# Optimization experiments

Hardware: AMD Instinct MI355X
Metric: run time of the kernel (lower is better)

Reference implementation:

```python
import jax, jax.numpy as jnp
import numpy as np

N = 50000      # nodes
E = 800000     # directed edges (before self-loops)
IN = 128       # in_channels
H = 4          # heads (layers 1,2)
C = 64         # hidden_channels per head
OUT = 512      # out_channels of final Linear
LEAKY_SLOPE = 0.2


def _gat_layer(x, src, dst, n, W, a_src, a_dst, b, concat):
    """PyG GATConv (v1): shared linear, additive attention, segment softmax over dst."""
    heads, ch = a_src.shape
    xl = (x @ W).reshape(n, heads, ch)                       # [N,H,C]
    as_n = jnp.sum(xl * a_src, axis=-1)                      # [N,H] alpha_src per node
    ad_n = jnp.sum(xl * a_dst, axis=-1)                      # [N,H] alpha_dst per node
    logits = jax.nn.leaky_relu(as_n[src] + ad_n[dst], LEAKY_SLOPE)  # [Etot,H]
    m = jax.lax.stop_gradient(jax.ops.segment_max(logits, dst, num_segments=n))
    p = jnp.exp(logits - m[dst])
    denom = jax.ops.segment_sum(p, dst, num_segments=n) + 1e-16
    alpha = p / denom[dst]                                   # segment softmax over incoming edges
    out = jax.ops.segment_sum(xl[src] * alpha[:, :, None], dst, num_segments=n)  # [N,H,C]
    out = out.reshape(n, heads * ch) if concat else out.mean(axis=1)
    return out + b


def setup_inputs() -> dict:
    key = jax.random.key(0)
    ks = jax.random.split(key, 16)

    def gl(k, shape, fan_in):
        return jax.random.normal(k, shape, dtype=jnp.float32) * np.float32(1.0 / np.sqrt(fan_in))

    x = jax.random.normal(ks[0], (N, IN), dtype=jnp.float32)
    edge_index = jax.random.randint(ks[1], (2, E), 0, N, dtype=jnp.int32)

    inp = {
        "x": x,
        "edge_index": edge_index,
        # layer 1: in -> H*C (concat)
        "W1": gl(ks[2], (IN, H * C), IN),
        "a_src1": gl(ks[3], (H, C), C),
        "a_dst1": gl(ks[4], (H, C), C),
        "b1": jnp.zeros((H * C,), jnp.float32),
        # layer 2: H*C -> H*C (concat)
        "W2": gl(ks[5], (H * C, H * C), H * C),
        "a_src2": gl(ks[6], (H, C), C),
        "a_dst2": gl(ks[7], (H, C), C),
        "b2": jnp.zeros((H * C,), jnp.float32),
        # layer 3: H*C -> C (1 head, no concat)
        "W3": gl(ks[8], (H * C, C), H * C),
        "a_src3": gl(ks[9], (1, C), C),
        "a_dst3": gl(ks[10], (1, C), C),
        "b3": jnp.zeros((C,), jnp.float32),
        # final fc: C -> OUT
        "Wfc": gl(ks[11], (C, OUT), C),
        "bfc": jnp.zeros((OUT,), jnp.float32),
    }
    return inp


def reference(x, edge_index, W1, a_src1, a_dst1, b1, W2, a_src2, a_dst2, b2,
              W3, a_src3, a_dst3, b3, Wfc, bfc):
    n = x.shape[0]
    loop = jnp.arange(n, dtype=edge_index.dtype)             # PyG GATConv adds self-loops
    src = jnp.concatenate([edge_index[0], loop])
    dst = jnp.concatenate([edge_index[1], loop])

    h = jax.nn.relu(_gat_layer(x, src, dst, n, W1, a_src1, a_dst1, b1, True))
    h = jax.nn.relu(_gat_layer(h, src, dst, n, W2, a_src2, a_dst2, b2, True))
    h = jax.nn.relu(_gat_layer(h, src, dst, n, W3, a_src3, a_dst3, b3, False))
    return jax.nn.relu(h @ Wfc + bfc)                        # [N, OUT]
```

## Files before the change

### kernel.cpp

```cpp
#include <hip/hip_runtime.h>
#include <cstdint>
#include <cstddef>

typedef unsigned short ushort_t;
typedef __bf16 bf16x8 __attribute__((ext_vector_type(8)));
typedef float f32x4 __attribute__((ext_vector_type(4)));

__device__ __forceinline__ float b2f(ushort_t u) {
    return __uint_as_float(((unsigned int)u) << 16);
}
__device__ __forceinline__ ushort_t f2b(float f) {
    __bf16 h = (__bf16)f;
    return *(ushort_t*)&h;
}
__device__ __forceinline__ float lo16(unsigned int u) { return __uint_as_float(u << 16); }
__device__ __forceinline__ float hi16(unsigned int u) { return __uint_as_float(u & 0xffff0000u); }
__device__ __forceinline__ unsigned int pack2(float a, float b) {
    return ((unsigned int)f2b(b) << 16) | (unsigned int)f2b(a);
}

__device__ __forceinline__ void stage8(const float* __restrict__ g, ushort_t* s) {
    float4 f0 = *(const float4*)g;
    float4 f1 = *(const float4*)(g + 4);
    union { ushort_t u[8]; uint4 v; } t;
    t.u[0] = f2b(f0.x); t.u[1] = f2b(f0.y); t.u[2] = f2b(f0.z); t.u[3] = f2b(f0.w);
    t.u[4] = f2b(f1.x); t.u[5] = f2b(f1.y); t.u[6] = f2b(f1.z); t.u[7] = f2b(f1.w);
    *(uint4*)s = t.v;
}
__device__ __forceinline__ void stage8(const ushort_t* __restrict__ g, ushort_t* s) {
    *(float4*)s = *(const float4*)g;
}

__device__ __forceinline__ void tr_seg(int id, const float* __restrict__ W,
                                       ushort_t* __restrict__ WT, int K, int N2) {
    int n = id / K, k = id - n * K;
    WT[id] = f2b(W[k * N2 + n]);
}
__global__ __launch_bounds__(256) void transpose_all_kernel(const float* __restrict__ W1,
                                                            const float* __restrict__ W2,
                                                            const float* __restrict__ W3,
                                                            const float* __restrict__ Wfc,
                                                            ushort_t* __restrict__ W1T,
                                                            ushort_t* __restrict__ W2T,
                                                            ushort_t* __restrict__ W3T,
                                                            ushort_t* __restrict__ WfcT,
                                                            int* __restrict__ deg, int n) {
    int id = blockIdx.x * 256 + threadIdx.x;
    if (id < n) deg[id] = 0;
    if (id < 32768) { tr_seg(id, W1, W1T, 128, 256); return; }
    id -= 32768;
    if (id < 65536) { tr_seg(id, W2, W2T, 256, 256); return; }
    id -= 65536;
    if (id < 16384) { tr_seg(id, W3, W3T, 256, 64); return; }
    id -= 16384;
    if (id < 32768) { tr_seg(id, Wfc, WfcT, 64, 512); return; }
}

__global__ __launch_bounds__(256) void degree_kernel(const int* __restrict__ ei_dst,
                                                     int* __restrict__ deg, int E, int Etot) {
    int e = blockIdx.x * 256 + threadIdx.x;
    if (e >= Etot) return;
    int d = (e < E) ? ei_dst[e] : (e - E);
    atomicAdd(&deg[d], 1);
}

__global__ __launch_bounds__(256) void partial_sum_kernel(const int* __restrict__ deg,
                                                          int* __restrict__ bsum, int n) {
    __shared__ int ws[4];
    int t = threadIdx.x;
    int i = blockIdx.x * 256 + t;
    int v = (i < n) ? deg[i] : 0;
#pragma unroll
    for (int off = 32; off; off >>= 1) v += __shfl_xor(v, off, 64);
    if ((t & 63) == 0) ws[t >> 6] = v;
    __syncthreads();
    if (t == 0) bsum[blockIdx.x] = ws[0] + ws[1] + ws[2] + ws[3];
}

__global__ __launch_bounds__(256) void scan_bsum_kernel(const int* __restrict__ bsum,
                                                        int* __restrict__ boff,
                                                        int* __restrict__ rowoff,
                                                        int nblk, int n) {
    __shared__ int sm[256];
    int t = threadIdx.x;
    int v = (t < nblk) ? bsum[t] : 0;
    sm[t] = v;
    __syncthreads();
#pragma unroll
    for (int off = 1; off < 256; off <<= 1) {
        int u = (t >= off) ? sm[t - off] : 0;
        __syncthreads();
        sm[t] += u;
        __syncthreads();
    }
    if (t < nblk) boff[t] = sm[t] - v;
    if (t == 255) rowoff[n] = sm[255];
}

__global__ __launch_bounds__(256) void block_scan_kernel(const int* __restrict__ deg,
                                                         const int* __restrict__ boff,
                                                         int* __restrict__ rowoff,
                                                         int* __restrict__ cursor, int n) {
    __shared__ int sm[256];
    int t = threadIdx.x;
    int i = blockIdx.x * 256 + t;
    int v = (i < n) ? deg[i] : 0;
    sm[t] = v;
    __syncthreads();
#pragma unroll
    for (int off = 1; off < 256; off <<= 1) {
        int u = (t >= off) ? sm[t - off] : 0;
        __syncthreads();
        sm[t] += u;
        __syncthreads();
    }
    if (i < n) {
        int r = boff[blockIdx.x] + sm[t] - v;
        rowoff[i] = r;
        cursor[i] = r;
    }
}

__global__ __launch_bounds__(256) void scatter_kernel(const int* __restrict__ ei_src,
                                                      const int* __restrict__ ei_dst,
                                                      int* __restrict__ cursor,
                                                      int* __restrict__ ssrc, int E, int Etot) {
    int e = blockIdx.x * 256 + threadIdx.x;
    if (e >= Etot) return;
    int s, d;
    if (e < E) { s = ei_src[e]; d = ei_dst[e]; } else { s = d = e - E; }
    int pos = atomicAdd(&cursor[d], 1);
    ssrc[pos] = s;
}

template <typename TA, int EPI>
__global__ __launch_bounds__(256) void gemm128_mfma(const TA* __restrict__ A,
                                                    const ushort_t* __restrict__ WT,
                                                    float* __restrict__ C,
                                                    ushort_t* __restrict__ Cb,
                                                    const float* __restrict__ bias,
                                                    const float* __restrict__ a_src,
                                                    const float* __restrict__ a_dst,
                                                    float* __restrict__ as_n,
                                                    float* __restrict__ ad_n,
                                                    int M, int K, int N2) {
    __shared__ ushort_t sA[128 * 32];
    __shared__ ushort_t sB[128 * 32];
    const int tid = threadIdx.x;
    const int wv = tid >> 6, lane = tid & 63;
    const int wr = wv >> 1, wc = wv & 1;
    const int quad = lane >> 4, l16 = lane & 15;
    const int bm = blockIdx.x * 128, bn = blockIdx.y * 128;
    const int sr0 = tid >> 2, sc = (tid & 3) * 8;
    const int sr1 = sr0 + 64;
    f32x4 acc[4][4] = {};

    int ga0 = bm + sr0; ga0 = ga0 < M ? ga0 : M - 1;
    int ga1 = bm + sr1; ga1 = ga1 < M ? ga1 : M - 1;
    const TA* pa0 = A + (size_t)ga0 * K + sc;
    const TA* pa1 = A + (size_t)ga1 * K + sc;
    const ushort_t* pb0 = WT + (size_t)(bn + sr0) * K + sc;
    const ushort_t* pb1 = WT + (size_t)(bn + sr1) * K + sc;

    for (int k0 = 0; k0 < K; k0 += 32) {
        stage8(pa0 + k0, sA + sr0 * 32 + sc);
        stage8(pa1 + k0, sA + sr1 * 32 + sc);
        stage8(pb0 + k0, sB + sr0 * 32 + sc);
        stage8(pb1 + k0, sB + sr1 * 32 + sc);
        __syncthreads();

        bf16x8 af[4], bfr[4];
#pragma unroll
        for (int m = 0; m < 4; m++)
            af[m] = *(const bf16x8*)(sA + (wr * 64 + m * 16 + l16) * 32 + quad * 8);
#pragma unroll
        for (int n = 0; n < 4; n++)
            bfr[n] = *(const bf16x8*)(sB + (wc * 64 + n * 16 + l16) * 32 + quad * 8);
#pragma unroll
        for (int m = 0; m < 4; m++)
#pragma unroll
            for (int n = 0; n < 4; n++)
                acc[m][n] = __builtin_amdgcn_mfma_f32_16x16x32_bf16(af[m], bfr[n], acc[m][n], 0, 0, 0);
        __syncthreads();
    }

#pragma unroll
    for (int n = 0; n < 4; n++) {
        int col = bn + wc * 64 + n * 16 + l16;
        float bv = (EPI == 1) ? bias[col] : 0.f;
#pragma unroll
        for (int m = 0; m < 4; m++) {
#pragma unroll
            for (int r = 0; r < 4; r++) {
                int row = bm + wr * 64 + m * 16 + quad * 4 + r;
                if (row < M) {
                    float v = acc[m][n][r];
                    if (EPI == 1) {
                        v += bv;
                        v = v > 0.f ? v : 0.f;
                        C[(size_t)row * N2 + col] = v;
                    } else {
                        Cb[(size_t)row * N2 + col] = f2b(v);
                    }
                }
            }
        }
    }

    if (EPI == 2) {
        const int head = blockIdx.y * 2 + wc;
        float asv[4], adv[4];
#pragma unroll
        for (int n = 0; n < 4; n++) {
            asv[n] = a_src[head * 64 + n * 16 + l16];
            adv[n] = a_dst[head * 64 + n * 16 + l16];
        }
        float ps[4][4] = {}, pd[4][4] = {};
#pragma unroll
        for (int n = 0; n < 4; n++)
#pragma unroll
            for (int m = 0; m < 4; m++)
#pragma unroll
                for (int r = 0; r < 4; r++) {
                    ps[m][r] += acc[m][n][r] * asv[n];
                    pd[m][r] += acc[m][n][r] * adv[n];
                }
#pragma unroll
        for (int off = 1; off < 16; off <<= 1)
#pragma unroll
            for (int m = 0; m < 4; m++)
#pragma unroll
                for (int r = 0; r < 4; r++) {
                    ps[m][r] += __shfl_xor(ps[m][r], off, 64);
                    pd[m][r] += __shfl_xor(pd[m][r], off, 64);
                }
        if (l16 == 0) {
#pragma unroll
            for (int m = 0; m < 4; m++)
#pragma unroll
                for (int r = 0; r < 4; r++) {
                    int row = bm + wr * 64 + m * 16 + quad * 4 + r;
                    if (row < M) {
                        as_n[row * 4 + head] = ps[m][r];
                        ad_n[row * 4 + head] = pd[m][r];
                    }
                }
        }
    }
}

__global__ __launch_bounds__(256) void gemm64_mfma(const ushort_t* __restrict__ A,
                                                   const ushort_t* __restrict__ WT,
                                                   ushort_t* __restrict__ Cb,
                                                   const float* __restrict__ a_src,
                                                   const float* __restrict__ a_dst,
                                                   float* __restrict__ as_n,
                                                   float* __restrict__ ad_n,
                                                   int M, int K, int N2) {
    __shared__ ushort_t sA[64 * 32];
    __shared__ ushort_t sB[64 * 32];
    const int tid = threadIdx.x;
    const int wv = tid >> 6, lane = tid & 63;
    const int quad = lane >> 4, l16 = lane & 15;
    const int bm = blockIdx.x * 64;
    const int srow = tid >> 2, skof = (tid & 3) * 8;
    f32x4 acc[4] = {};

    int gm = bm + srow;
    gm = gm < M ? gm : M - 1;
    const ushort_t* pa = A + (size_t)gm * K + skof;
    const ushort_t* pb = WT + (size_t)srow * K + skof;

    for (int k0 = 0; k0 < K; k0 += 32) {
        *(float4*)(sA + srow * 32 + skof) = *(const float4*)(pa + k0);
        *(float4*)(sB + srow * 32 + skof) = *(const float4*)(pb + k0);
        __syncthreads();

        bf16x8 af = *(const bf16x8*)(sA + (wv * 16 + l16) * 32 + quad * 8);
#pragma unroll
        for (int j = 0; j < 4; j++) {
            bf16x8 bf = *(const bf16x8*)(sB + (j * 16 + l16) * 32 + quad * 8);
            acc[j] = __builtin_amdgcn_mfma_f32_16x16x32_bf16(af, bf, acc[j], 0, 0, 0);
        }
        __syncthreads();
    }

#pragma unroll
    for (int j = 0; j < 4; j++) {
        int col = j * 16 + l16;
#pragma unroll
        for (int r = 0; r < 4; r++) {
            int row = bm + wv * 16 + quad * 4 + r;
            if (row < M) Cb[(size_t)row * N2 + col] = f2b(acc[j][r]);
        }
    }

    float asv[4], adv[4];
#pragma unroll
    for (int j = 0; j < 4; j++) {
        asv[j] = a_src[j * 16 + l16];
        adv[j] = a_dst[j * 16 + l16];
    }
    float ps[4] = {}, pd[4] = {};
#pragma unroll
    for (int j = 0; j < 4; j++)
#pragma unroll
        for (int r = 0; r < 4; r++) {
            ps[r] += acc[j][r] * asv[j];
            pd[r] += acc[j][r] * adv[j];
        }
#pragma unroll
    for (int off = 1; off < 16; off <<= 1)
#pragma unroll
        for (int r = 0; r < 4; r++) {
            ps[r] += __shfl_xor(ps[r], off, 64);
            pd[r] += __shfl_xor(pd[r], off, 64);
        }
    if (l16 == 0) {
#pragma unroll
        for (int r = 0; r < 4; r++) {
            int row = bm + wv * 16 + quad * 4 + r;
            if (row < M) {
                as_n[row] = ps[r];
                ad_n[row] = pd[r];
            }
        }
    }
}

template <int CH>
__global__ __launch_bounds__(256) void aggregate_kernel(const ushort_t* __restrict__ xl,
                                                        const float* __restrict__ as_n,
                                                        const float* __restrict__ ad_n,
                                                        const int* __restrict__ rowoff,
                                                        const int* __restrict__ ssrc,
                                                        const float* __restrict__ bias,
                                                        ushort_t* __restrict__ hout, int N) {
    const int tid = threadIdx.x;
    const int wv = tid >> 6, lane = tid & 63;
    const uint4* xv = (const uint4*)xl;
    if (CH == 256) {
        const int hw = lane >> 5, l32 = lane & 31;
        const int dd = blockIdx.x * 8 + wv * 2 + hw;
        if (dd >= N) return;
        const int h = l32 >> 3;
        const int r0 = rowoff[dd], r1 = rowoff[dd + 1];
        const float adv = ad_n[dd * 4 + h];
        float a0 = 0, a1 = 0, a2 = 0, a3 = 0, a4 = 0, a5 = 0, a6 = 0, a7 = 0, den = 0;
        for (int i = r0; i < r1; i += 8) {
            int s[8];
            float g[8];
            uint4 u[8];
#pragma unroll
            for (int j = 0; j < 8; j++) {
                int t = i + j;
                s[j] = ssrc[t < r1 ? t : r0];
            }
#pragma unroll
            for (int j = 0; j < 8; j++) g[j] = as_n[s[j] * 4 + h];
#pragma unroll
            for (int j = 0; j < 8; j++) u[j] = xv[(size_t)s[j] * 32 + l32];
#pragma unroll
            for (int j = 0; j < 8; j++) {
                float lg = g[j] + adv;
                lg = lg > 0.f ? lg : 0.2f * lg;
                float p = (i + j < r1) ? __expf(lg) : 0.f;
                den += p;
                a0 += p * lo16(u[j].x); a1 += p * hi16(u[j].x);
                a2 += p * lo16(u[j].y); a3 += p * hi16(u[j].y);
                a4 += p * lo16(u[j].z); a5 += p * hi16(u[j].z);
                a6 += p * lo16(u[j].w); a7 += p * hi16(u[j].w);
            }
        }
        float di = 1.f / (den + 1e-16f);
        float4 b0 = ((const float4*)bias)[l32 * 2];
        float4 b1 = ((const float4*)bias)[l32 * 2 + 1];
        float v0 = a0 * di + b0.x, v1 = a1 * di + b0.y;
        float v2 = a2 * di + b0.z, v3 = a3 * di + b0.w;
        float v4 = a4 * di + b1.x, v5 = a5 * di + b1.y;
        float v6 = a6 * di + b1.z, v7 = a7 * di + b1.w;
        v0 = v0 > 0.f ? v0 : 0.f; v1 = v1 > 0.f ? v1 : 0.f;
        v2 = v2 > 0.f ? v2 : 0.f; v3 = v3 > 0.f ? v3 : 0.f;
        v4 = v4 > 0.f ? v4 : 0.f; v5 = v5 > 0.f ? v5 : 0.f;
        v6 = v6 > 0.f ? v6 : 0.f; v7 = v7 > 0.f ? v7 : 0.f;
        uint4 o;
        o.x = pack2(v0, v1); o.y = pack2(v2, v3);
        o.z = pack2(v4, v5); o.w = pack2(v6, v7);
        ((uint4*)hout)[(size_t)dd * 32 + l32] = o;
    } else {
        const int grp = lane >> 3, l8 = lane & 7;
        const int dd = blockIdx.x * 32 + wv * 8 + grp;
        if (dd >= N) return;
        const int r0 = rowoff[dd], r1 = rowoff[dd + 1];
        const float adv = ad_n[dd];
        float a0 = 0, a1 = 0, a2 = 0, a3 = 0, a4 = 0, a5 = 0, a6 = 0, a7 = 0, den = 0;
        for (int i = r0; i < r1; i += 8) {
            int s[8];
            float g[8];
            uint4 u[8];
#pragma unroll
            for (int j = 0; j < 8; j++) {
                int t = i + j;
                s[j] = ssrc[t < r1 ? t : r0];
            }
#pragma unroll
            for (int j = 0; j < 8; j++) g[j] = as_n[s[j]];
#pragma unroll
            for (int j = 0; j < 8; j++) u[j] = xv[(size_t)s[j] * 8 + l8];
#pragma unroll
            for (int j = 0; j < 8; j++) {
                float lg = g[j] + adv;
                lg = lg > 0.f ? lg : 0.2f * lg;
                float p = (i + j < r1) ? __expf(lg) : 0.f;
                den += p;
                a0 += p * lo16(u[j].x); a1 += p * hi16(u[j].x);
                a2 += p * lo16(u[j].y); a3 += p * hi16(u[j].y);
                a4 += p * lo16(u[j].z); a5 += p * hi16(u[j].z);
                a6 += p * lo16(u[j].w); a7 += p * hi16(u[j].w);
            }
        }
        float di = 1.f / (den + 1e-16f);
        float4 b0 = ((const float4*)bias)[l8 * 2];
        float4 b1 = ((const float4*)bias)[l8 * 2 + 1];
        float v0 = a0 * di + b0.x, v1 = a1 * di + b0.y;
        float v2 = a2 * di + b0.z, v3 = a3 * di + b0.w;
        float v4 = a4 * di + b1.x, v5 = a5 * di + b1.y;
        float v6 = a6 * di + b1.z, v7 = a7 * di + b1.w;
        v0 = v0 > 0.f ? v0 : 0.f; v1 = v1 > 0.f ? v1 : 0.f;
        v2 = v2 > 0.f ? v2 : 0.f; v3 = v3 > 0.f ? v3 : 0.f;
        v4 = v4 > 0.f ? v4 : 0.f; v5 = v5 > 0.f ? v5 : 0.f;
        v6 = v6 > 0.f ? v6 : 0.f; v7 = v7 > 0.f ? v7 : 0.f;
        uint4 o;
        o.x = pack2(v0, v1); o.y = pack2(v2, v3);
        o.z = pack2(v4, v5); o.w = pack2(v6, v7);
        ((uint4*)hout)[(size_t)dd * 8 + l8] = o;
    }
}

extern "C" void kernel_launch(void* const* d_in, const int* in_sizes, int n_in,
                              void* d_out, int out_size, void* d_ws, size_t ws_size,
                              hipStream_t stream) {
    const int N = in_sizes[0] / 128;
    const int E = in_sizes[1] / 2;
    const int Etot = E + N;

    const float* x = (const float*)d_in[0];
    const int* ei = (const int*)d_in[1];
    const int* ei_src = ei;
    const int* ei_dst = ei + E;
    float* out = (float*)d_out;

    const float* as1 = (const float*)d_in[3];
    const float* ad1 = (const float*)d_in[4];
    const float* b1  = (const float*)d_in[5];
    const float* as2 = (const float*)d_in[7];
    const float* ad2 = (const float*)d_in[8];
    const float* b2  = (const float*)d_in[9];
    const float* as3 = (const float*)d_in[11];
    const float* ad3 = (const float*)d_in[12];
    const float* b3  = (const float*)d_in[13];
    const float* bfc = (const float*)d_in[15];

    ushort_t* bufX = (ushort_t*)d_ws;
    ushort_t* bufH = bufX + (size_t)N * 256;
    ushort_t* W1T  = bufH + (size_t)N * 256;
    ushort_t* W2T  = W1T + 32768;
    ushort_t* W3T  = W2T + 65536;
    ushort_t* WfcT = W3T + 16384;
    float* asn = (float*)(WfcT + 32768);
    float* adn = asn + (size_t)N * 4;
    int* deg    = (int*)(adn + (size_t)N * 4);
    int* rowoff = deg + N;
    int* cursor = rowoff + N + 1;
    int* ssrc   = cursor + N;
    int* bsum   = ssrc + Etot;
    int* boff   = bsum + 256;

    transpose_all_kernel<<<576, 256, 0, stream>>>((const float*)d_in[2], (const float*)d_in[6],
                                                  (const float*)d_in[10], (const float*)d_in[14],
                                                  W1T, W2T, W3T, WfcT, deg, N);

    int eb = (Etot + 255) / 256;
    degree_kernel<<<eb, 256, 0, stream>>>(ei_dst, deg, E, Etot);
    const int NBLK = (N + 255) / 256;
    partial_sum_kernel<<<NBLK, 256, 0, stream>>>(deg, bsum, N);
    scan_bsum_kernel<<<1, 256, 0, stream>>>(bsum, boff, rowoff, NBLK, N);
    block_scan_kernel<<<NBLK, 256, 0, stream>>>(deg, boff, rowoff, cursor, N);
    scatter_kernel<<<eb, 256, 0, stream>>>(ei_src, ei_dst, cursor, ssrc, E, Etot);

    const int MB128 = (N + 127) / 128;
    const int MB64 = (N + 63) / 64;
    int nb8 = (N + 7) / 8;
    int nb32 = (N + 31) / 32;

    gemm128_mfma<float, 2><<<dim3(MB128, 2), 256, 0, stream>>>(
        x, W1T, nullptr, bufX, nullptr, as1, ad1, asn, adn, N, 128, 256);
    aggregate_kernel<256><<<nb8, 256, 0, stream>>>(bufX, asn, adn, rowoff, ssrc, b1, bufH, N);

    gemm128_mfma<ushort_t, 2><<<dim3(MB128, 2), 256, 0, stream>>>(
        bufH, W2T, nullptr, bufX, nullptr, as2, ad2, asn, adn, N, 256, 256);
    aggregate_kernel<256><<<nb8, 256, 0, stream>>>(bufX, asn, adn, rowoff, ssrc, b2, bufH, N);

    gemm64_mfma<<<dim3(MB64, 1), 256, 0, stream>>>(bufH, W3T, bufX, as3, ad3, asn, adn, N, 256, 64);
    aggregate_kernel<64><<<nb32, 256, 0, stream>>>(bufX, asn, adn, rowoff, ssrc, b3, bufH, N);

    gemm128_mfma<ushort_t, 1><<<dim3(MB128, 4), 256, 0, stream>>>(
        bufH, WfcT, out, nullptr, bfc, nullptr, nullptr, nullptr, nullptr, N, 64, 512);
}
```

Measured before the change: 483.3 us.

## Store GAT features slice-major and aggregate one 32-channel slice per block

The projection GEMM now writes bf16 features in a slice-major layout (8 slices of 32 channels, each an N x 32 array), and the 256-channel aggregation is split so that each block handles a single slice for 8 destination nodes. Edges are spread across 8 lane slots, and the partial sums are combined with cross-lane shuffles. The goal is a smaller gather working set per block (64 bytes per source row per slice), which should fit better in L2/MALL and spread edge parallelism across lanes. In exchange, the attention logits and exp are recomputed 8 times per edge (once per slice instead of once per head), the shuffle reduction adds work, and the feature gathers are scattered across 8 separate slices.

Result: slower. 541.1 us (+12.0%).

```diff
diff --git a/kernel.cpp b/kernel.cpp
--- a/kernel.cpp
+++ b/kernel.cpp
@@ -133,7 +133,7 @@
     ssrc[pos] = s;
 }
 
-template <typename TA, int EPI>
+template <typename TA, int EPI, bool SMAJ>
 __global__ __launch_bounds__(256) void gemm128_mfma(const TA* __restrict__ A,
                                                     const ushort_t* __restrict__ WT,
                                                     float* __restrict__ C,
@@ -199,6 +199,8 @@
                         v += bv;
                         v = v > 0.f ? v : 0.f;
                         C[(size_t)row * N2 + col] = v;
+                    } else if (SMAJ) {
+                        Cb[((size_t)(col >> 5) * M + row) * 32 + (col & 31)] = f2b(v);
                     } else {
                         Cb[(size_t)row * N2 + col] = f2b(v);
                     }
@@ -328,53 +330,50 @@
     }
 }
 
-template <int CH>
-__global__ __launch_bounds__(256) void aggregate_kernel(const ushort_t* __restrict__ xl,
-                                                        const float* __restrict__ as_n,
-                                                        const float* __restrict__ ad_n,
-                                                        const int* __restrict__ rowoff,
-                                                        const int* __restrict__ ssrc,
-                                                        const float* __restrict__ bias,
-                                                        ushort_t* __restrict__ hout, int N) {
+__global__ __launch_bounds__(256) void aggregate256_slice_kernel(
+    const ushort_t* __restrict__ xs, const float* __restrict__ as_n,
+    const float* __restrict__ ad_n, const int* __restrict__ rowoff,
+    const int* __restrict__ ssrc, const float* __restrict__ bias,
+    ushort_t* __restrict__ hout, int N) {
+    const int bid = blockIdx.x;
+    const int slice = bid & 7;
+    const int db = bid >> 3;
     const int tid = threadIdx.x;
     const int wv = tid >> 6, lane = tid & 63;
-    const uint4* xv = (const uint4*)xl;
-    if (CH == 256) {
-        const int hw = lane >> 5, l32 = lane & 31;
-        const int dd = blockIdx.x * 8 + wv * 2 + hw;
-        if (dd >= N) return;
-        const int h = l32 >> 3;
-        const int r0 = rowoff[dd], r1 = rowoff[dd + 1];
-        const float adv = ad_n[dd * 4 + h];
-        float a0 = 0, a1 = 0, a2 = 0, a3 = 0, a4 = 0, a5 = 0, a6 = 0, a7 = 0, den = 0;
-        for (int i = r0; i < r1; i += 8) {
-            int s[8];
-            float g[8];
-            uint4 u[8];
-#pragma unroll
-            for (int j = 0; j < 8; j++) {
-                int t = i + j;
-                s[j] = ssrc[t < r1 ? t : r0];
-            }
-#pragma unroll
-            for (int j = 0; j < 8; j++) g[j] = as_n[s[j] * 4 + h];
-#pragma unroll
-            for (int j = 0; j < 8; j++) u[j] = xv[(size_t)s[j] * 32 + l32];
-#pragma unroll
-            for (int j = 0; j < 8; j++) {
-                float lg = g[j] + adv;
-                lg = lg > 0.f ? lg : 0.2f * lg;
-                float p = (i + j < r1) ? __expf(lg) : 0.f;
-                den += p;
-                a0 += p * lo16(u[j].x); a1 += p * hi16(u[j].x);
-                a2 += p * lo16(u[j].y); a3 += p * hi16(u[j].y);
-                a4 += p * lo16(u[j].z); a5 += p * hi16(u[j].z);
-                a6 += p * lo16(u[j].w); a7 += p * hi16(u[j].w);
-            }
-        }
+    const int half = lane >> 5, l32 = lane & 31;
+    const int slot = l32 >> 2, sub = l32 & 3;
+    const int dd = db * 8 + wv * 2 + half;
+    if (dd >= N) return;
+    const int h = slice >> 1;
+    const int r0 = rowoff[dd], r1 = rowoff[dd + 1];
+    const float adv = ad_n[dd * 4 + h];
+    const uint4* xv = (const uint4*)xs;
+    const size_t sbase = (size_t)slice * N;
+    float a0 = 0, a1 = 0, a2 = 0, a3 = 0, a4 = 0, a5 = 0, a6 = 0, a7 = 0, den = 0;
+    for (int i = r0 + slot; i < r1; i += 8) {
+        int s = ssrc[i];
+        float lg = as_n[s * 4 + h] + adv;
+        lg = lg > 0.f ? lg : 0.2f * lg;
+        float p = __expf(lg);
+        uint4 u = xv[(sbase + s) * 4 + sub];
+        den += p;
+        a0 += p * lo16(u.x); a1 += p * hi16(u.x);
+        a2 += p * lo16(u.y); a3 += p * hi16(u.y);
+        a4 += p * lo16(u.z); a5 += p * hi16(u.z);
+        a6 += p * lo16(u.w); a7 += p * hi16(u.w);
+    }
+#pragma unroll
+    for (int off = 4; off < 32; off <<= 1) {
+        a0 += __shfl_xor(a0, off, 64); a1 += __shfl_xor(a1, off, 64);
+        a2 += __shfl_xor(a2, off, 64); a3 += __shfl_xor(a3, off, 64);
+        a4 += __shfl_xor(a4, off, 64); a5 += __shfl_xor(a5, off, 64);
+        a6 += __shfl_xor(a6, off, 64); a7 += __shfl_xor(a7, off, 64);
+        den += __shfl_xor(den, off, 64);
+    }
+    if (slot == 0) {
         float di = 1.f / (den + 1e-16f);
-        float4 b0 = ((const float4*)bias)[l32 * 2];
-        float4 b1 = ((const float4*)bias)[l32 * 2 + 1];
+        const float4* bp = (const float4*)(bias + slice * 32 + sub * 8);
+        float4 b0 = bp[0], b1 = bp[1];
         float v0 = a0 * di + b0.x, v1 = a1 * di + b0.y;
         float v2 = a2 * di + b0.z, v3 = a3 * di + b0.w;
         float v4 = a4 * di + b1.x, v5 = a5 * di + b1.y;
@@ -386,55 +385,66 @@
         uint4 o;
         o.x = pack2(v0, v1); o.y = pack2(v2, v3);
         o.z = pack2(v4, v5); o.w = pack2(v6, v7);
-        ((uint4*)hout)[(size_t)dd * 32 + l32] = o;
-    } else {
-        const int grp = lane >> 3, l8 = lane & 7;
-        const int dd = blockIdx.x * 32 + wv * 8 + grp;
-        if (dd >= N) return;
-        const int r0 = rowoff[dd], r1 = rowoff[dd + 1];
-        const float adv = ad_n[dd];
-        float a0 = 0, a1 = 0, a2 = 0, a3 = 0, a4 = 0, a5 = 0, a6 = 0, a7 = 0, den = 0;
-        for (int i = r0; i < r1; i += 8) {
-            int s[8];
-            float g[8];
-            uint4 u[8];
-#pragma unroll
-            for (int j = 0; j < 8; j++) {
-                int t = i + j;
-                s[j] = ssrc[t < r1 ? t : r0];
-            }
-#pragma unroll
-            for (int j = 0; j < 8; j++) g[j] = as_n[s[j]];
-#pragma unroll
-            for (int j = 0; j < 8; j++) u[j] = xv[(size_t)s[j] * 8 + l8];
-#pragma unroll
-            for (int j = 0; j < 8; j++) {
-                float lg = g[j] + adv;
-                lg = lg > 0.f ? lg : 0.2f * lg;
-                float p = (i + j < r1) ? __expf(lg) : 0.f;
-                den += p;
-                a0 += p * lo16(u[j].x); a1 += p * hi16(u[j].x);
-                a2 += p * lo16(u[j].y); a3 += p * hi16(u[j].y);
-                a4 += p * lo16(u[j].z); a5 += p * hi16(u[j].z);
-                a6 += p * lo16(u[j].w); a7 += p * hi16(u[j].w);
-            }
-        }
-        float di = 1.f / (den + 1e-16f);
-        float4 b0 = ((const float4*)bias)[l8 * 2];
-        float4 b1 = ((const float4*)bias)[l8 * 2 + 1];
-        float v0 = a0 * di + b0.x, v1 = a1 * di + b0.y;
-        float v2 = a2 * di + b0.z, v3 = a3 * di + b0.w;
-        float v4 = a4 * di + b1.x, v5 = a5 * di + b1.y;
-        float v6 = a6 * di + b1.z, v7 = a7 * di + b1.w;
-        v0 = v0 > 0.f ? v0 : 0.f; v1 = v1 > 0.f ? v1 : 0.f;
-        v2 = v2 > 0.f ? v2 : 0.f; v3 = v3 > 0.f ? v3 : 0.f;
-        v4 = v4 > 0.f ? v4 : 0.f; v5 = v5 > 0.f ? v5 : 0.f;
-        v6 = v6 > 0.f ? v6 : 0.f; v7 = v7 > 0.f ? v7 : 0.f;
-        uint4 o;
-        o.x = pack2(v0, v1); o.y = pack2(v2, v3);
-        o.z = pack2(v4, v5); o.w = pack2(v6, v7);
-        ((uint4*)hout)[(size_t)dd * 8 + l8] = o;
-    }
+        ((uint4*)hout)[(size_t)dd * 32 + slice * 4 + sub] = o;
+    }
+}
+
+__global__ __launch_bounds__(256) void aggregate64_kernel(const ushort_t* __restrict__ xl,
+                                                          const float* __restrict__ as_n,
+                                                          const float* __restrict__ ad_n,
+                                                          const int* __restrict__ rowoff,
+                                                          const int* __restrict__ ssrc,
+                                                          const float* __restrict__ bias,
+                                                          ushort_t* __restrict__ hout, int N) {
+    const int tid = threadIdx.x;
+    const int wv = tid >> 6, lane = tid & 63;
+    const uint4* xv = (const uint4*)xl;
+    const int grp = lane >> 3, l8 = lane & 7;
+    const int dd = blockIdx.x * 32 + wv * 8 + grp;
+    if (dd >= N) return;
+    const int r0 = rowoff[dd], r1 = rowoff[dd + 1];
+    const float adv = ad_n[dd];
+    float a0 = 0, a1 = 0, a2 = 0, a3 = 0, a4 = 0, a5 = 0, a6 = 0, a7 = 0, den = 0;
+    for (int i = r0; i < r1; i += 8) {
+        int s[8];
+        float g[8];
+        uint4 u[8];
+#pragma unroll
+        for (int j = 0; j < 8; j++) {
+            int t = i + j;
+            s[j] = ssrc[t < r1 ? t : r0];
+        }
+#pragma unroll
+        for (int j = 0; j < 8; j++) g[j] = as_n[s[j]];
+#pragma unroll
+        for (int j = 0; j < 8; j++) u[j] = xv[(size_t)s[j] * 8 + l8];
+#pragma unroll
+        for (int j = 0; j < 8; j++) {
+            float lg = g[j] + adv;
+            lg = lg > 0.f ? lg : 0.2f * lg;
+            float p = (i + j < r1) ? __expf(lg) : 0.f;
+            den += p;
+            a0 += p * lo16(u[j].x); a1 += p * hi16(u[j].x);
+            a2 += p * lo16(u[j].y); a3 += p * hi16(u[j].y);
+            a4 += p * lo16(u[j].z); a5 += p * hi16(u[j].z);
+            a6 += p * lo16(u[j].w); a7 += p * hi16(u[j].w);
+        }
+    }
+    float di = 1.f / (den + 1e-16f);
+    float4 b0 = ((const float4*)bias)[l8 * 2];
+    float4 b1 = ((const float4*)bias)[l8 * 2 + 1];
+    float v0 = a0 * di + b0.x, v1 = a1 * di + b0.y;
+    float v2 = a2 * di + b0.z, v3 = a3 * di + b0.w;
+    float v4 = a4 * di + b1.x, v5 = a5 * di + b1.y;
+    float v6 = a6 * di + b1.z, v7 = a7 * di + b1.w;
+    v0 = v0 > 0.f ? v0 : 0.f; v1 = v1 > 0.f ? v1 : 0.f;
+    v2 = v2 > 0.f ? v2 : 0.f; v3 = v3 > 0.f ? v3 : 0.f;
+    v4 = v4 > 0.f ? v4 : 0.f; v5 = v5 > 0.f ? v5 : 0.f;
+    v6 = v6 > 0.f ? v6 : 0.f; v7 = v7 > 0.f ? v7 : 0.f;
+    uint4 o;
+    o.x = pack2(v0, v1); o.y = pack2(v2, v3);
+    o.z = pack2(v4, v5); o.w = pack2(v6, v7);
+    ((uint4*)hout)[(size_t)dd * 8 + l8] = o;
 }
 
 extern "C" void kernel_launch(void* const* d_in, const int* in_sizes, int n_in,
@@ -490,20 +500,20 @@
 
     const int MB128 = (N + 127) / 128;
     const int MB64 = (N + 63) / 64;
-    int nb8 = (N + 7) / 8;
+    const int nbS = ((N + 7) / 8) * 8;
     int nb32 = (N + 31) / 32;
 
-    gemm128_mfma<float, 2><<<dim3(MB128, 2), 256, 0, stream>>>(
+    gemm128_mfma<float, 2, true><<<dim3(MB128, 2), 256, 0, stream>>>(
         x, W1T, nullptr, bufX, nullptr, as1, ad1, asn, adn, N, 128, 256);
-    aggregate_kernel<256><<<nb8, 256, 0, stream>>>(bufX, asn, adn, rowoff, ssrc, b1, bufH, N);
-
-    gemm128_mfma<ushort_t, 2><<<dim3(MB128, 2), 256, 0, stream>>>(
+    aggregate256_slice_kernel<<<nbS, 256, 0, stream>>>(bufX, asn, adn, rowoff, ssrc, b1, bufH, N);
+
+    gemm128_mfma<ushort_t, 2, true><<<dim3(MB128, 2), 256, 0, stream>>>(
         bufH, W2T, nullptr, bufX, nullptr, as2, ad2, asn, adn, N, 256, 256);
-    aggregate_kernel<256><<<nb8, 256, 0, stream>>>(bufX, asn, adn, rowoff, ssrc, b2, bufH, N);
+    aggregate256_slice_kernel<<<nbS, 256, 0, stream>>>(bufX, asn, adn, rowoff, ssrc, b2, bufH, N);
 
     gemm64_mfma<<<dim3(MB64, 1), 256, 0, stream>>>(bufH, W3T, bufX, as3, ad3, asn, adn, N, 256, 64);
-    aggregate_kernel<64><<<nb32, 256, 0, stream>>>(bufX, asn, adn, rowoff, ssrc, b3, bufH, N);
-
-    gemm128_mfma<ushort_t, 1><<<dim3(MB128, 4), 256, 0, stream>>>(
+    aggregate64_kernel<<<nb32, 256, 0, stream>>>(bufX, asn, adn, rowoff, ssrc, b3, bufH, N);
+
+    gemm128_mfma<ushort_t, 1, false><<<dim3(MB128, 4), 256, 0, stream>>>(
         bufH, WfcT, out, nullptr, bfc, nullptr, nullptr, nullptr, nullptr, N, 64, 512);
 }
```
